# Kernel tuning notes

Measured on AMD Instinct MI355X. Metric: run time of the kernel, lower is better.

The kernel has to match this reference:

```python
import jax, jax.numpy as jnp
import numpy as np

B, L, E, MODES = 32, 1024, 512, 64


def setup_inputs() -> dict:
    key = jax.random.key(0)
    k1, k2, k3 = jax.random.split(key, 3)
    scale = 1.0 / (E * E)
    q = jax.random.normal(k1, (B, L, E), dtype=jnp.float32)
    # torch.rand(..., dtype=cfloat) -> real and imag each uniform [0,1)
    w_real = scale * jax.random.uniform(k2, (E, E, MODES), dtype=jnp.float32)
    w_imag = scale * jax.random.uniform(k3, (E, E, MODES), dtype=jnp.float32)
    return {"q": q, "w_real": w_real, "w_imag": w_imag}


def reference(q, w_real, w_imag):
    # mode_select_method='lowest': index = [0..MODES-1], sorted
    index = jnp.arange(MODES)
    x = jnp.transpose(q, (0, 2, 1))            # [B, E, L]
    x_ft = jnp.fft.rfft(x, axis=-1)            # [B, E, L//2+1] complex
    xg = x_ft[:, :, index]                     # gather selected modes [B, E, M]
    W = w_real + 1j * w_imag                   # [E_in, E_out, M] complex
    # fused batched complex GEMM over all modes (replaces per-mode loop)
    out_modes = jnp.einsum('bhm,him->bim', xg, W)  # [B, E, M]
    F = L // 2 + 1
    out_ft = jnp.zeros((B, E, F), dtype=out_modes.dtype)
    # original writes results at positions wi = 0..M-1 (loop index), not at `index`
    out_ft = out_ft.at[:, :, :MODES].set(out_modes)
    x_out = jnp.fft.irfft(out_ft, n=L, axis=-1)    # [B, E, L] real
    return jnp.transpose(x_out, (0, 2, 1))         # [B, L, E]
```

## Files before the change

### kernel.cpp

```cpp
#include <hip/hip_runtime.h>
#include <math.h>

#define LQ 1024
#define EQ 512
#define BQ 32
#define MQ 64

static constexpr int BCHUNK = LQ * EQ;

typedef short short8 __attribute__((ext_vector_type(8)));
typedef float f32x4 __attribute__((ext_vector_type(4)));
typedef unsigned short ushort_t;

union FragI { int i[4]; int4 v; short8 s; };

__device__ __forceinline__ void gload16(const float* g, float* l) {
    __builtin_amdgcn_global_load_lds(
        (const __attribute__((address_space(1))) void*)g,
        (__attribute__((address_space(3))) void*)l, 16, 0, 0);
}

__device__ inline char* sx_ptr(float* dout, int arr, int m, int b, int h) {
    unsigned G = ((unsigned)arr << 20) + ((unsigned)m << 14) +
                 ((unsigned)(h >> 5) << 10) + ((unsigned)b << 5) + (unsigned)(h & 31);
    unsigned z = G >> 19, w = G & 524287u;
    return (char*)(dout + (size_t)z * BCHUNK + 262144) + (size_t)w * 2;
}

__device__ inline void split2(float a, float b, unsigned& hi, unsigned& lo) {
    unsigned ua = __float_as_uint(a), ub = __float_as_uint(b);
    unsigned ha = ua & 0xFFFF0000u, hb = ub & 0xFFFF0000u;
    hi = (ua >> 16) | hb;
    float la = a - __uint_as_float(ha);
    float lb = b - __uint_as_float(hb);
    lo = (__float_as_uint(la) >> 16) | (__float_as_uint(lb) & 0xFFFF0000u);
}

__device__ inline void split1(float x, ushort_t& hi, ushort_t& lo) {
    unsigned u = __float_as_uint(x);
    hi = (ushort_t)(u >> 16);
    float r = x - __uint_as_float(u & 0xFFFF0000u);
    lo = (ushort_t)(__float_as_uint(r) >> 16);
}

__global__ __launch_bounds__(256) void k_trig(unsigned* __restrict__ BFhi,
                                              unsigned* __restrict__ BFlo,
                                              float* __restrict__ dout) {
    int idx = blockIdx.x * 256 + threadIdx.x;
    int l = idx >> 6, m = idx & 63;
    int tt = (l * m) & (LQ - 1);
    float ang = (float)tt * 6.135923151542565e-03f;
    float s, c;
    sincosf(ang, &s, &c);
    float coef = (m == 0 ? 1.0f : 2.0f) * (1.0f / (float)LQ);
    float b0 = coef * c;
    float b1 = (m == 0) ? 0.0f : (-2.0f / (float)LQ) * s;
    unsigned hi, lo;
    split2(b0, b1, hi, lo);
    {
        int lt = l >> 4, kb = m >> 4, kgb = (m & 15) >> 2;
        int lane = kgb * 16 + (l & 15);
        int u = lt * 1024 + kb * 256 + lane * 4 + (m & 3);
        BFhi[u] = hi;
        BFlo[u] = lo;
    }
    ushort_t* THs = (ushort_t*)dout;
    ushort_t* TLs = (ushort_t*)(dout + 65536);
    int ks = l >> 5, kg = (l >> 3) & 3, j = l & 7;
    int mt = m >> 3;
    int lane0 = kg * 16 + 2 * (m & 7);
    ushort_t ch, cl, sh, sl;
    split1(c, ch, cl);
    split1(-s, sh, sl);
    int u0 = ((ks * 8 + mt) * 64 + lane0) * 8 + j;
    THs[u0] = ch;  TLs[u0] = cl;
    THs[u0 + 8] = sh;  TLs[u0 + 8] = sl;
}

#define MM(A, B, C) C = __builtin_amdgcn_mfma_f32_16x16x32_bf16(A, B, C, 0, 0, 0)

__global__ __launch_bounds__(512, 4) void k_dft4(const float* __restrict__ q,
                                                 float* __restrict__ dout) {
    __shared__ float qs[2 * 2048];
    const int t    = threadIdx.x;
    const int wave = t >> 6;
    const int lane = t & 63;
    const int a    = wave & 3;
    const int ht   = wave >> 2;
    const int b    = blockIdx.x >> 4;
    const int hg   = blockIdx.x & 15;
    const int hbase = hg * 32;
    const int col  = lane & 15;
    const int kg   = lane >> 4;
    const float* qb = q + (size_t)b * BCHUNK;
    const int4* TH4 = (const int4*)dout;
    const int4* TL4 = (const int4*)(dout + 65536);

    f32x4 acc[2] = {{0.f, 0.f, 0.f, 0.f}, {0.f, 0.f, 0.f, 0.f}};
    const int lp = wave * 8 + (lane >> 3);
    const int hq = 4 * (lane & 7);

    gload16(qb + (size_t)lp * EQ + hbase + hq, &qs[wave * 256]);

    int cur = 0;
    for (int cc = 0; cc < 16; ++cc) {
        __syncthreads();
        FragI ah[2][2], al[2][2];
#pragma unroll
        for (int ksl = 0; ksl < 2; ++ksl)
#pragma unroll
            for (int ti = 0; ti < 2; ++ti) {
                int idx = ((cc * 2 + ksl) * 8 + 2 * a + ti) * 64 + lane;
                ah[ksl][ti].v = TH4[idx];
                al[ksl][ti].v = TL4[idx];
            }
        if (cc < 15)
            gload16(qb + (size_t)((cc + 1) * 64 + lp) * EQ + hbase + hq,
                    &qs[(cur ^ 1) * 2048 + wave * 256]);
#pragma unroll
        for (int ksl = 0; ksl < 2; ++ksl) {
            float v[8];
#pragma unroll
            for (int j = 0; j < 8; ++j)
                v[j] = qs[cur * 2048 + (ksl * 32 + kg * 8 + j) * 32 + ht * 16 + col];
            FragI bhiF, bloF;
#pragma unroll
            for (int k2 = 0; k2 < 4; ++k2) {
                unsigned h_, l_;
                split2(v[2 * k2], v[2 * k2 + 1], h_, l_);
                bhiF.i[k2] = (int)h_;
                bloF.i[k2] = (int)l_;
            }
#pragma unroll
            for (int ti = 0; ti < 2; ++ti) {
                MM(ah[ksl][ti].s, bhiF.s, acc[ti]);
                MM(ah[ksl][ti].s, bloF.s, acc[ti]);
                MM(al[ksl][ti].s, bhiF.s, acc[ti]);
            }
        }
        cur ^= 1;
    }
    const int h = hbase + ht * 16 + col;
#pragma unroll
    for (int ti = 0; ti < 2; ++ti) {
        int mt = 2 * a + ti;
        int mA = mt * 8 + kg * 2;
#pragma unroll
        for (int mi = 0; mi < 2; ++mi) {
            float xr = acc[ti][2 * mi];
            float xi = acc[ti][2 * mi + 1];
            ushort_t rh, rl, ih_, il_;
            split1(xr, rh, rl);
            split1(xi, ih_, il_);
            int m = mA + mi;
            *(ushort_t*)sx_ptr(dout, 0, m, b, h) = rh;
            *(ushort_t*)sx_ptr(dout, 1, m, b, h) = rl;
            *(ushort_t*)sx_ptr(dout, 2, m, b, h) = ih_;
            *(ushort_t*)sx_ptr(dout, 3, m, b, h) = il_;
        }
    }
}

__global__ __launch_bounds__(512, 4) void k_modes7(const float* __restrict__ wreal,
                                                   const float* __restrict__ wimag,
                                                   float* __restrict__ dout) {
    __shared__ float Wlds[16384];
    const int t    = threadIdx.x;
    const int wave = t >> 6;
    const int lane = t & 63;
    const int blk  = blockIdx.x;
    const int hs   = blk >> 7;
    const int mc   = (blk >> 5) & 3;
    const int it   = blk & 31;
    const int i0   = it * 16;
    const int m0   = mc * 16;
    const int col  = lane & 15;
    const int kg   = lane >> 4;
    const int hbase = hs * 128;

    const char* xp0 = sx_ptr(dout, 0, m0 + 2 * wave, col, hbase + kg * 8);

    f32x4 zero4 = {0.f, 0.f, 0.f, 0.f};
    f32x4 acc[2][2][2];
#pragma unroll
    for (int a = 0; a < 2; ++a)
#pragma unroll
        for (int bq = 0; bq < 2; ++bq)
#pragma unroll
            for (int c = 0; c < 2; ++c) acc[a][bq][c] = zero4;

    FragI xA[4], xB[4];
    short8 aW[2][2];
    short8 nW[2];

#define LDX(BUF, MI, NT, KK)                                                  \
    {                                                                         \
        const char* xpm_ = xp0 + (size_t)(MI) * 32768 +                       \
                           (size_t)(KK) * 2048 + (size_t)(NT) * 1024;         \
        BUF[0].v = *(const int4*)(xpm_);                                      \
        BUF[1].v = *(const int4*)(xpm_ + 4194304);                            \
        BUF[2].v = *(const int4*)(xpm_ + 2 * 4194304);                        \
        BUF[3].v = *(const int4*)(xpm_ + 3 * 4194304);                        \
    }

#define READW(MI)                                                             \
    {                                                                         \
        const int mloc_ = 2 * wave + (MI);                                    \
        const int mb4_ = mloc_ >> 2;                                          \
        const int mo_ = mloc_ & 3;                                            \
        _Pragma("unroll")                                                     \
        for (int part = 0; part < 2; ++part) {                                \
            float v[8];                                                       \
            _Pragma("unroll")                                                 \
            for (int j = 0; j < 8; ++j)                                       \
                v[j] = Wlds[part * 8192 + (kg * 8 + j) * 256 + col * 16 +     \
                            ((mb4_ ^ kg) << 2) + mo_];                        \
            FragI hiF, loF;                                                   \
            _Pragma("unroll")                                                 \
            for (int k2 = 0; k2 < 4; ++k2) {                                  \
                unsigned h_, l_;                                              \
                split2(v[2 * k2], v[2 * k2 + 1], h_, l_);                     \
                hiF.i[k2] = (int)h_;                                          \
                loF.i[k2] = (int)l_;                                          \
            }                                                                 \
            aW[part][0] = hiF.s;                                              \
            aW[part][1] = loF.s;                                              \
        }                                                                     \
        FragI th_, tl_, nh_, nl_;                                             \
        th_.s = aW[1][0]; tl_.s = aW[1][1];                                   \
        _Pragma("unroll")                                                     \
        for (int k2 = 0; k2 < 4; ++k2) {                                      \
            nh_.i[k2] = th_.i[k2] ^ 0x80008000;                               \
            nl_.i[k2] = tl_.i[k2] ^ 0x80008000;                               \
        }                                                                     \
        nW[0] = nh_.s;                                                        \
        nW[1] = nl_.s;                                                        \
    }

#define MMG(MI, NT, BUF)                                                      \
    MM(aW[0][0], BUF[0].s, acc[MI][0][NT]);                                   \
    MM(aW[0][0], BUF[1].s, acc[MI][0][NT]);                                   \
    MM(aW[0][1], BUF[0].s, acc[MI][0][NT]);                                   \
    MM(nW[0],    BUF[2].s, acc[MI][0][NT]);                                   \
    MM(nW[0],    BUF[3].s, acc[MI][0][NT]);                                   \
    MM(nW[1],    BUF[2].s, acc[MI][0][NT]);                                   \
    MM(aW[0][0], BUF[2].s, acc[MI][1][NT]);                                   \
    MM(aW[0][0], BUF[3].s, acc[MI][1][NT]);                                   \
    MM(aW[0][1], BUF[2].s, acc[MI][1][NT]);                                   \
    MM(aW[1][0], BUF[0].s, acc[MI][1][NT]);                                   \
    MM(aW[1][0], BUF[1].s, acc[MI][1][NT]);                                   \
    MM(aW[1][1], BUF[0].s, acc[MI][1][NT]);

    LDX(xA, 0, 0, 0);
    for (int kk = 0; kk < 4; ++kk) {
        __syncthreads();
#pragma unroll
        for (int r = 0; r < 8; ++r) {
            const int W64 = r * 8 + wave;
            const int part = W64 >> 5;
            const int h = W64 & 31;
            const int hx = (h >> 3) & 3;
            const float* srcb = part ? wimag : wreal;
            const float* src = srcb +
                (size_t)(hbase + kk * 32 + h) * 32768 +
                (size_t)(i0 + (lane >> 2)) * 64 + m0 + 4 * ((lane & 3) ^ hx);
            gload16(src, &Wlds[W64 * 256]);
        }
        __syncthreads();
        LDX(xB, 0, 1, kk);
        READW(0);
        MMG(0, 0, xA);
        LDX(xA, 1, 0, kk);
        MMG(0, 1, xB);
        READW(1);
        LDX(xB, 1, 1, kk);
        MMG(1, 0, xA);
        if (kk < 3) LDX(xA, 0, 0, kk + 1);
        MMG(1, 1, xB);
    }
#undef LDX
#undef READW
#undef MMG
#pragma unroll
    for (int mi = 0; mi < 2; ++mi)
#pragma unroll
        for (int part = 0; part < 2; ++part)
#pragma unroll
            for (int nt = 0; nt < 2; ++nt) {
                int bb = nt * 16 + col;
                int c = 2 * (m0 + 2 * wave + mi) + part;
                f32x4 vv = acc[mi][part][nt];
                float4 o = make_float4(vv.x, vv.y, vv.z, vv.w);
                *(float4*)&dout[(size_t)bb * BCHUNK + (size_t)hs * 65536 +
                                (size_t)c * EQ + i0 + kg * 4] = o;
            }
}

__global__ __launch_bounds__(256) void k_inv3(const unsigned* __restrict__ BFhi,
                                              const unsigned* __restrict__ BFlo,
                                              float* __restrict__ dout) {
    __shared__ unsigned Bf[4096];
    const int t    = threadIdx.x;
    const int wave = t >> 6;
    const int lane = t & 63;
    const int b    = blockIdx.x >> 4;
    const int it   = blockIdx.x & 15;
    const int i0   = it * 32;
    float* base = dout + (size_t)b * BCHUNK;

#pragma unroll
    for (int r = 0; r < 8; ++r) {
        int idx = r * 256 + t;
        int il = idx & 31, cp = idx >> 5;
        int c0 = 2 * cp;
        const float* p0 = base + (size_t)c0 * EQ + i0 + il;
        float s0 = p0[0] + p0[65536] + p0[2 * 65536] + p0[3 * 65536];
        const float* p1 = p0 + EQ;
        float s1 = p1[0] + p1[65536] + p1[2 * 65536] + p1[3 * 65536];
        unsigned hi, lo;
        split2(s0, s1, hi, lo);
        int nt = il >> 4, i_loc = il & 15;
        int kb = c0 >> 5, kg = (c0 & 31) >> 3, jp = (c0 & 7) >> 1;
        int u = (nt * 4 + kb) * 256 + (kg * 16 + i_loc) * 4 + jp;
        Bf[u] = hi;
        Bf[2048 + u] = lo;
    }
    __syncthreads();
    FragI bh[2][4], bl[2][4];
#pragma unroll
    for (int nt = 0; nt < 2; ++nt)
#pragma unroll
        for (int kb = 0; kb < 4; ++kb) {
            bh[nt][kb].v = *(const int4*)&Bf[(nt * 4 + kb) * 256 + lane * 4];
            bl[nt][kb].v = *(const int4*)&Bf[2048 + (nt * 4 + kb) * 256 + lane * 4];
        }
    for (int r = 0; r < 16; ++r) {
        int lt = wave + 4 * r;
        FragI ah[4], al[4];
#pragma unroll
        for (int kb = 0; kb < 4; ++kb) {
            ah[kb].v = *(const int4*)&BFhi[lt * 1024 + kb * 256 + lane * 4];
            al[kb].v = *(const int4*)&BFlo[lt * 1024 + kb * 256 + lane * 4];
        }
        f32x4 a0 = {0.f, 0.f, 0.f, 0.f}, a1 = {0.f, 0.f, 0.f, 0.f};
#pragma unroll
        for (int kb = 0; kb < 4; ++kb) {
            MM(ah[kb].s, bh[0][kb].s, a0);
            MM(ah[kb].s, bl[0][kb].s, a0);
            MM(al[kb].s, bh[0][kb].s, a0);
            MM(ah[kb].s, bh[1][kb].s, a1);
            MM(ah[kb].s, bl[1][kb].s, a1);
            MM(al[kb].s, bh[1][kb].s, a1);
        }
        int lrow = lt * 16 + (lane >> 4) * 4;
        int icol = i0 + (lane & 15);
#pragma unroll
        for (int j = 0; j < 4; ++j) {
            base[(size_t)(lrow + j) * EQ + icol]      = a0[j];
            base[(size_t)(lrow + j) * EQ + icol + 16] = a1[j];
        }
    }
}
#undef MM

extern "C" void kernel_launch(void* const* d_in, const int* in_sizes, int n_in,
                              void* d_out, int out_size, void* d_ws, size_t ws_size,
                              hipStream_t stream) {
    const float* q  = (const float*)d_in[0];
    const float* wr = (const float*)d_in[1];
    const float* wi = (const float*)d_in[2];
    float* out = (float*)d_out;
    unsigned* BFhi = (unsigned*)d_ws;
    unsigned* BFlo = BFhi + 65536;

    hipLaunchKernelGGL(k_trig,   dim3(256), dim3(256), 0, stream, BFhi, BFlo, out);
    hipLaunchKernelGGL(k_dft4,   dim3(512), dim3(512), 0, stream, q, out);
    hipLaunchKernelGGL(k_modes7, dim3(512), dim3(512), 0, stream, wr, wi, out);
    hipLaunchKernelGGL(k_inv3,   dim3(512), dim3(256), 0, stream, BFhi, BFlo, out);
}
```

Before: 143.4 us.

## Retile mode GEMM to 64 outputs x 4 modes and prefetch weights

The mode-mixing kernel now gives each block 64 output channels by 4 modes instead of 16 by 16. Each W row load is then one contiguous 16-byte chunk per lane, covering the 4 modes, which replaces the strided, XOR-swizzled gathers. The W fragments for both mode sub-tiles are read from LDS once per k-step as float2 pairs and split to bf16 before the barrier. The next k-step's W tile is staged asynchronously while the MFMAs run, overlapping global-to-LDS traffic with compute. The cost is more live fragment registers, and any LDS bank-conflict effects of the new layout are left unaddressed.

Result: slower. 177.5 us (+23.8%).

```diff
diff --git a/kernel.cpp b/kernel.cpp
--- a/kernel.cpp
+++ b/kernel.cpp
@@ -161,24 +161,26 @@
     }
 }
 
-__global__ __launch_bounds__(512, 4) void k_modes7(const float* __restrict__ wreal,
+__global__ __launch_bounds__(512, 4) void k_modes8(const float* __restrict__ wreal,
                                                    const float* __restrict__ wimag,
                                                    float* __restrict__ dout) {
     __shared__ float Wlds[16384];
     const int t    = threadIdx.x;
     const int wave = t >> 6;
     const int lane = t & 63;
+    const int isub = wave >> 1;
+    const int mw   = wave & 1;
     const int blk  = blockIdx.x;
     const int hs   = blk >> 7;
-    const int mc   = (blk >> 5) & 3;
-    const int it   = blk & 31;
-    const int i0   = it * 16;
-    const int m0   = mc * 16;
+    const int mg   = (blk >> 3) & 15;
+    const int it   = blk & 7;
+    const int i0   = it * 64;
+    const int m0   = mg * 4;
     const int col  = lane & 15;
     const int kg   = lane >> 4;
     const int hbase = hs * 128;
 
-    const char* xp0 = sx_ptr(dout, 0, m0 + 2 * wave, col, hbase + kg * 8);
+    const char* xp0 = sx_ptr(dout, 0, m0 + 2 * mw, col, hbase + kg * 8);
 
     f32x4 zero4 = {0.f, 0.f, 0.f, 0.f};
     f32x4 acc[2][2][2];
@@ -190,8 +192,21 @@
             for (int c = 0; c < 2; ++c) acc[a][bq][c] = zero4;
 
     FragI xA[4], xB[4];
-    short8 aW[2][2];
-    short8 nW[2];
+    short8 aW[2][2][2];
+
+#define STAGE(KK)                                                             \
+    {                                                                         \
+        _Pragma("unroll")                                                     \
+        for (int r = 0; r < 8; ++r) {                                         \
+            const int W64_ = r * 8 + wave;                                    \
+            const int part_ = W64_ >> 5;                                      \
+            const int h_ = W64_ & 31;                                         \
+            const float* src_ = (part_ ? wimag : wreal) +                     \
+                (size_t)(hbase + (KK) * 32 + h_) * 32768 +                    \
+                (size_t)(i0 + lane) * 64 + m0;                                \
+            gload16(src_, &Wlds[W64_ * 256]);                                 \
+        }                                                                     \
+    }
 
 #define LDX(BUF, MI, NT, KK)                                                  \
     {                                                                         \
@@ -203,83 +218,70 @@
         BUF[3].v = *(const int4*)(xpm_ + 3 * 4194304);                        \
     }
 
-#define READW(MI)                                                             \
+#define MMG(MI, NT, BUF)                                                      \
     {                                                                         \
-        const int mloc_ = 2 * wave + (MI);                                    \
-        const int mb4_ = mloc_ >> 2;                                          \
-        const int mo_ = mloc_ & 3;                                            \
-        _Pragma("unroll")                                                     \
-        for (int part = 0; part < 2; ++part) {                                \
-            float v[8];                                                       \
-            _Pragma("unroll")                                                 \
-            for (int j = 0; j < 8; ++j)                                       \
-                v[j] = Wlds[part * 8192 + (kg * 8 + j) * 256 + col * 16 +     \
-                            ((mb4_ ^ kg) << 2) + mo_];                        \
-            FragI hiF, loF;                                                   \
-            _Pragma("unroll")                                                 \
-            for (int k2 = 0; k2 < 4; ++k2) {                                  \
-                unsigned h_, l_;                                              \
-                split2(v[2 * k2], v[2 * k2 + 1], h_, l_);                     \
-                hiF.i[k2] = (int)h_;                                          \
-                loF.i[k2] = (int)l_;                                          \
-            }                                                                 \
-            aW[part][0] = hiF.s;                                              \
-            aW[part][1] = loF.s;                                              \
-        }                                                                     \
         FragI th_, tl_, nh_, nl_;                                             \
-        th_.s = aW[1][0]; tl_.s = aW[1][1];                                   \
+        th_.s = aW[MI][1][0]; tl_.s = aW[MI][1][1];                           \
         _Pragma("unroll")                                                     \
         for (int k2 = 0; k2 < 4; ++k2) {                                      \
             nh_.i[k2] = th_.i[k2] ^ 0x80008000;                               \
             nl_.i[k2] = tl_.i[k2] ^ 0x80008000;                               \
         }                                                                     \
-        nW[0] = nh_.s;                                                        \
-        nW[1] = nl_.s;                                                        \
-    }
-
-#define MMG(MI, NT, BUF)                                                      \
-    MM(aW[0][0], BUF[0].s, acc[MI][0][NT]);                                   \
-    MM(aW[0][0], BUF[1].s, acc[MI][0][NT]);                                   \
-    MM(aW[0][1], BUF[0].s, acc[MI][0][NT]);                                   \
-    MM(nW[0],    BUF[2].s, acc[MI][0][NT]);                                   \
-    MM(nW[0],    BUF[3].s, acc[MI][0][NT]);                                   \
-    MM(nW[1],    BUF[2].s, acc[MI][0][NT]);                                   \
-    MM(aW[0][0], BUF[2].s, acc[MI][1][NT]);                                   \
-    MM(aW[0][0], BUF[3].s, acc[MI][1][NT]);                                   \
-    MM(aW[0][1], BUF[2].s, acc[MI][1][NT]);                                   \
-    MM(aW[1][0], BUF[0].s, acc[MI][1][NT]);                                   \
-    MM(aW[1][0], BUF[1].s, acc[MI][1][NT]);                                   \
-    MM(aW[1][1], BUF[0].s, acc[MI][1][NT]);
-
+        MM(aW[MI][0][0], BUF[0].s, acc[MI][0][NT]);                           \
+        MM(aW[MI][0][0], BUF[1].s, acc[MI][0][NT]);                           \
+        MM(aW[MI][0][1], BUF[0].s, acc[MI][0][NT]);                           \
+        MM(nh_.s,        BUF[2].s, acc[MI][0][NT]);                           \
+        MM(nh_.s,        BUF[3].s, acc[MI][0][NT]);                           \
+        MM(nl_.s,        BUF[2].s, acc[MI][0][NT]);                           \
+        MM(aW[MI][0][0], BUF[2].s, acc[MI][1][NT]);                           \
+        MM(aW[MI][0][0], BUF[3].s, acc[MI][1][NT]);                           \
+        MM(aW[MI][0][1], BUF[2].s, acc[MI][1][NT]);                           \
+        MM(aW[MI][1][0], BUF[0].s, acc[MI][1][NT]);                           \
+        MM(aW[MI][1][0], BUF[1].s, acc[MI][1][NT]);                           \
+        MM(aW[MI][1][1], BUF[0].s, acc[MI][1][NT]);                           \
+    }
+
+    STAGE(0);
     LDX(xA, 0, 0, 0);
+    __syncthreads();
     for (int kk = 0; kk < 4; ++kk) {
+#pragma unroll
+        for (int part = 0; part < 2; ++part) {
+            float2 v2[8];
+#pragma unroll
+            for (int j = 0; j < 8; ++j)
+                v2[j] = *(const float2*)&Wlds[(part * 32 + kg * 8 + j) * 256 +
+                                              (isub * 16 + col) * 4 + 2 * mw];
+#pragma unroll
+            for (int mi = 0; mi < 2; ++mi) {
+                FragI hiF, loF;
+#pragma unroll
+                for (int k2 = 0; k2 < 4; ++k2) {
+                    float a_ = mi ? v2[2 * k2].y : v2[2 * k2].x;
+                    float b_ = mi ? v2[2 * k2 + 1].y : v2[2 * k2 + 1].x;
+                    unsigned h_, l_;
+                    split2(a_, b_, h_, l_);
+                    hiF.i[k2] = (int)h_;
+                    loF.i[k2] = (int)l_;
+                }
+                aW[mi][part][0] = hiF.s;
+                aW[mi][part][1] = loF.s;
+            }
+        }
         __syncthreads();
-#pragma unroll
-        for (int r = 0; r < 8; ++r) {
-            const int W64 = r * 8 + wave;
-            const int part = W64 >> 5;
-            const int h = W64 & 31;
-            const int hx = (h >> 3) & 3;
-            const float* srcb = part ? wimag : wreal;
-            const float* src = srcb +
-                (size_t)(hbase + kk * 32 + h) * 32768 +
-                (size_t)(i0 + (lane >> 2)) * 64 + m0 + 4 * ((lane & 3) ^ hx);
-            gload16(src, &Wlds[W64 * 256]);
-        }
-        __syncthreads();
+        if (kk < 3) STAGE(kk + 1);
         LDX(xB, 0, 1, kk);
-        READW(0);
         MMG(0, 0, xA);
         LDX(xA, 1, 0, kk);
         MMG(0, 1, xB);
-        READW(1);
         LDX(xB, 1, 1, kk);
         MMG(1, 0, xA);
         if (kk < 3) LDX(xA, 0, 0, kk + 1);
         MMG(1, 1, xB);
-    }
+        __syncthreads();
+    }
+#undef STAGE
 #undef LDX
-#undef READW
 #undef MMG
 #pragma unroll
     for (int mi = 0; mi < 2; ++mi)
@@ -288,11 +290,11 @@
 #pragma unroll
             for (int nt = 0; nt < 2; ++nt) {
                 int bb = nt * 16 + col;
-                int c = 2 * (m0 + 2 * wave + mi) + part;
+                int c = 2 * (m0 + 2 * mw + mi) + part;
                 f32x4 vv = acc[mi][part][nt];
                 float4 o = make_float4(vv.x, vv.y, vv.z, vv.w);
                 *(float4*)&dout[(size_t)bb * BCHUNK + (size_t)hs * 65536 +
-                                (size_t)c * EQ + i0 + kg * 4] = o;
+                                (size_t)c * EQ + i0 + isub * 16 + kg * 4] = o;
             }
 }
 
@@ -375,6 +377,6 @@
 
     hipLaunchKernelGGL(k_trig,   dim3(256), dim3(256), 0, stream, BFhi, BFlo, out);
     hipLaunchKernelGGL(k_dft4,   dim3(512), dim3(512), 0, stream, q, out);
-    hipLaunchKernelGGL(k_modes7, dim3(512), dim3(512), 0, stream, wr, wi, out);
+    hipLaunchKernelGGL(k_modes8, dim3(512), dim3(512), 0, stream, wr, wi, out);
     hipLaunchKernelGGL(k_inv3,   dim3(512), dim3(256), 0, stream, BFhi, BFlo, out);
 }
```
